# Kernel optimization log

Hardware: AMD Instinct MI355X
Metric: run time of the kernel (lower is better)

Reference implementation:

```python
import jax, jax.numpy as jnp
import numpy as np

B, CIN, H = 8192, 512, 2048  # batch, in_channels, hidden_channels


def _ln(x, g, b, eps=1e-5):
    m = jnp.mean(x, axis=-1, keepdims=True)
    v = jnp.var(x, axis=-1, keepdims=True)
    return (x - m) * jax.lax.rsqrt(v + eps) * g + b


def setup_inputs() -> dict:
    key = jax.random.key(0)
    ks = jax.random.split(key, 16)
    d = {
        'x': jax.random.normal(ks[0], (B, 1, CIN), jnp.float32),
        'h': jax.random.normal(ks[1], (B, H), jnp.float32),
        'c': jax.random.normal(ks[2], (B, H), jnp.float32),
        # input_proj: in_channels -> hidden
        'W_proj': jax.random.normal(ks[3], (H, CIN), jnp.float32) / np.sqrt(CIN),
        'b_proj': jnp.zeros((H,), jnp.float32),
        # layerNorm over concat(x_proj, h) of width 2H
        'g_ln': jnp.ones((2 * H,), jnp.float32),
        'b_ln': jnp.zeros((2 * H,), jnp.float32),
        # cell_norm / hidden_norm
        'g_cn': jnp.ones((H,), jnp.float32),
        'b_cn': jnp.zeros((H,), jnp.float32),
        'g_hn': jnp.ones((H,), jnp.float32),
        'b_hn': jnp.zeros((H,), jnp.float32),
    }
    for name, k in zip(['f', 'i', 'c2', 'o'], ks[4:8]):
        d[f'W_{name}'] = jax.random.normal(k, (H, 2 * H), jnp.float32) / np.sqrt(2 * H)
        d[f'b_{name}'] = jnp.zeros((H,), jnp.float32)
        d[f'g_{name}'] = jnp.ones((H,), jnp.float32)
        d[f'beta_{name}'] = jnp.zeros((H,), jnp.float32)
    return d


def reference(x, h, c, W_proj, b_proj, g_ln, b_ln, g_cn, b_cn, g_hn, b_hn,
              W_f, b_f, g_f, beta_f, W_i, b_i, g_i, beta_i,
              W_c2, b_c2, g_c2, beta_c2, W_o, b_o, g_o, beta_o):
    # x: [B,1,CIN] -> squeeze, project to hidden width (CIN != H branch)
    xp = x[:, 0, :] @ W_proj.T + b_proj                      # [B,H]
    combined = jnp.concatenate([xp, h], axis=-1)             # [B,2H]
    combined = jnp.tanh(_ln(combined, g_ln, b_ln))           # activation = tanh
    # four gate blocks: Linear(2H->H) + LayerNorm (dropout = identity in eval)
    f = jax.nn.sigmoid(_ln(combined @ W_f.T + b_f, g_f, beta_f))
    i = jax.nn.sigmoid(_ln(combined @ W_i.T + b_i, g_i, beta_i))
    o = jax.nn.sigmoid(_ln(combined @ W_o.T + b_o, g_o, beta_o))
    cc = jnp.tanh(_ln(combined @ W_c2.T + b_c2, g_c2, beta_c2))
    next_cell = _ln(f * c + i * cc, g_cn, b_cn)
    next_hidden = jnp.tanh(_ln(o * jnp.tanh(next_cell), g_hn, b_hn))
    # original returns (next_hidden, (next_hidden, next_cell)); stack the two states
    return jnp.stack([next_hidden, next_cell])               # [2,B,H]
```

## Files before the change

kernel.cpp:

```cpp
#include <hip/hip_runtime.h>
#include <stdint.h>


typedef __attribute__((ext_vector_type(8))) short short8;
typedef __attribute__((ext_vector_type(4))) float f32x4;

__device__ __forceinline__ unsigned short f2bf(float x) {
  union { float f; uint32_t u; } v; v.f = x;
  uint32_t r = v.u + 0x7FFFu + ((v.u >> 16) & 1u);
  return (unsigned short)(r >> 16);
}
__device__ __forceinline__ float bf2f(unsigned short u) {
  union { uint32_t u; float f; } v; v.u = ((uint32_t)u) << 16; return v.f;
}
__device__ __forceinline__ void unpack8(uint4 p, float* o) {
  uint32_t w[4] = {p.x, p.y, p.z, p.w};
#pragma unroll
  for (int k = 0; k < 4; k++) {
    o[2*k]   = bf2f((unsigned short)(w[k] & 0xffffu));
    o[2*k+1] = bf2f((unsigned short)(w[k] >> 16));
  }
}
__device__ __forceinline__ uint4 pack8(const float* s) {
  uint4 r;
  r.x = (uint32_t)f2bf(s[0]) | ((uint32_t)f2bf(s[1]) << 16);
  r.y = (uint32_t)f2bf(s[2]) | ((uint32_t)f2bf(s[3]) << 16);
  r.z = (uint32_t)f2bf(s[4]) | ((uint32_t)f2bf(s[5]) << 16);
  r.w = (uint32_t)f2bf(s[6]) | ((uint32_t)f2bf(s[7]) << 16);
  return r;
}
__device__ __forceinline__ float tanh_fast(float x) {
  x = fminf(fmaxf(x, -15.f), 15.f);
  float e = __expf(-2.f * x);
  return (1.f - e) / (1.f + e);
}
__device__ __forceinline__ float sigmoid_fast(float x) {
  return 1.f / (1.f + __expf(-x));
}

__global__ __launch_bounds__(256)
void cvt_all(const float* __restrict__ x, const float* __restrict__ Wp,
             const float* __restrict__ Wf, const float* __restrict__ Wi,
             const float* __restrict__ Wc2, const float* __restrict__ Wo,
             unsigned short* __restrict__ xbf, unsigned short* __restrict__ wpbf,
             unsigned short* __restrict__ Wcat) {
  const int blk = blockIdx.x;
  const float* src;
  unsigned short* dst;
  int i;
  if (blk < 2048) {
    src = x; dst = xbf; i = blk * 256 + threadIdx.x;
  } else if (blk < 2560) {
    src = Wp; dst = wpbf; i = (blk - 2048) * 256 + threadIdx.x;
  } else {
    int b2 = blk - 2560;
    int w = b2 >> 12;
    src = (w == 0) ? Wf : (w == 1) ? Wi : (w == 2) ? Wc2 : Wo;
    dst = Wcat + (size_t)w * 8388608;
    i = (b2 & 4095) * 256 + threadIdx.x;
  }
  const float4* s4 = (const float4*)src;
  float4 a = s4[2*i], b = s4[2*i+1];
  float t[8] = {a.x,a.y,a.z,a.w,b.x,b.y,b.z,b.w};
  ((uint4*)dst)[i] = pack8(t);
}

#define MFMA16(a, b, c) __builtin_amdgcn_mfma_f32_16x16x32_bf16((a), (b), (c), 0, 0, 0)
#define GLDS16(g, l)                                                         \
  __builtin_amdgcn_global_load_lds(                                          \
      (const __attribute__((address_space(1))) void*)(g),                    \
      (__attribute__((address_space(3))) void*)(l), 16, 0, 0)

__global__ __launch_bounds__(512, 2)
void gemm_8ph(const unsigned short* __restrict__ A,
              const unsigned short* __restrict__ Bw,
              const float* __restrict__ b0, const float* __restrict__ b1,
              const float* __restrict__ b2, const float* __restrict__ b3,
              unsigned short* __restrict__ C,
              int M, int N, int K) {
  __shared__ __align__(16) unsigned short As[2][2][128][64];
  __shared__ __align__(16) unsigned short Bs[2][2][128][64];

  const int tid  = threadIdx.x;
  const int lane = tid & 63;
  const int wv   = tid >> 6;
  const int wm   = wv >> 2;
  const int wn   = wv & 3;

  const int nbx = N >> 8;
  const int nwg = (M >> 8) * nbx;
  const int bid = blockIdx.x;
  const int cpx = nwg >> 3;
  const int tile = (nwg & 7) ? bid : (bid & 7) * cpx + (bid >> 3);
  const int bm = (tile / nbx) << 8;
  const int bn = (tile % nbx) << 8;

  const int srow = wv * 8 + (lane >> 3);
  const int schk = (lane & 7) ^ (lane >> 3);
  const unsigned short* ag = A  + (size_t)(bm + srow) * K + schk * 8;
  const unsigned short* bg = Bw + (size_t)(bn + srow) * K + schk * 8;

#define STAGE_A(t, h)                                                        \
  do {                                                                       \
    GLDS16(ag + (size_t)((h) * 128)      * K + (t) * 64,                     \
           &As[(t) & 1][(h)][wv * 8][0]);                                    \
    GLDS16(ag + (size_t)((h) * 128 + 64) * K + (t) * 64,                     \
           &As[(t) & 1][(h)][64 + wv * 8][0]);                               \
  } while (0)
#define STAGE_B(t, h)                                                        \
  do {                                                                       \
    GLDS16(bg + (size_t)((h) * 128)      * K + (t) * 64,                     \
           &Bs[(t) & 1][(h)][wv * 8][0]);                                    \
    GLDS16(bg + (size_t)((h) * 128 + 64) * K + (t) * 64,                     \
           &Bs[(t) & 1][(h)][64 + wv * 8][0]);                               \
  } while (0)

  const int cl = lane & 15, q = lane >> 4;
  const int ard0 = cl * 64 + ((q       ^ (cl & 7)) * 8);
  const int ard1 = cl * 64 + (((4 | q) ^ (cl & 7)) * 8);
  const int brd0 = ((wn & 1) * 64 + cl) * 64 + ((q       ^ (cl & 7)) * 8);
  const int brd1 = ((wn & 1) * 64 + cl) * 64 + (((4 | q) ^ (cl & 7)) * 8);
  const unsigned short* pa0 = &As[0][wm][0][0];
  const unsigned short* pa1 = &As[1][wm][0][0];
  const unsigned short* pb0 = &Bs[0][wn >> 1][0][0];
  const unsigned short* pb1 = &Bs[1][wn >> 1][0][0];

  STAGE_A(0, 0); STAGE_A(0, 1); STAGE_B(0, 0); STAGE_B(0, 1);
  STAGE_A(1, 0);

  f32x4 acc[8][4];
#pragma unroll
  for (int r = 0; r < 8; ++r)
#pragma unroll
    for (int j = 0; j < 4; ++j) acc[r][j] = (f32x4){0.f, 0.f, 0.f, 0.f};

  asm volatile("s_waitcnt vmcnt(2)");
  __builtin_amdgcn_s_barrier();

  short8 af[8], bv[4];
  const int NI = K >> 7;

  for (int i = 0; i < NI; ++i) {
    const int t = 2 * i;
    const bool pf = (i + 1 < NI);

#pragma unroll
    for (int r = 0; r < 8; ++r) af[r] = *(const short8*)(pa0 + ard0 + r * 1024);
    bv[0] = *(const short8*)(pb0 + brd0);
    bv[1] = *(const short8*)(pb0 + brd0 + 1024);
    STAGE_A(t + 1, 1);
    __builtin_amdgcn_s_barrier();
    asm volatile("s_waitcnt lgkmcnt(0)");
    __builtin_amdgcn_s_setprio(1);
#pragma unroll
    for (int r = 0; r < 8; ++r) {
      acc[r][0] = MFMA16(af[r], bv[0], acc[r][0]);
      acc[r][1] = MFMA16(af[r], bv[1], acc[r][1]);
    }
    __builtin_amdgcn_s_setprio(0);
    __builtin_amdgcn_s_barrier();

    bv[2] = *(const short8*)(pb0 + brd0 + 2048);
    bv[3] = *(const short8*)(pb0 + brd0 + 3072);
    STAGE_B(t + 1, 0);
    __builtin_amdgcn_s_barrier();
    asm volatile("s_waitcnt lgkmcnt(0)");
    __builtin_amdgcn_s_setprio(1);
#pragma unroll
    for (int r = 0; r < 8; ++r) {
      acc[r][2] = MFMA16(af[r], bv[2], acc[r][2]);
      acc[r][3] = MFMA16(af[r], bv[3], acc[r][3]);
    }
    __builtin_amdgcn_s_setprio(0);
    __builtin_amdgcn_s_barrier();

#pragma unroll
    for (int r = 0; r < 8; ++r) af[r] = *(const short8*)(pa0 + ard1 + r * 1024);
    bv[0] = *(const short8*)(pb0 + brd1);
    bv[1] = *(const short8*)(pb0 + brd1 + 1024);
    STAGE_B(t + 1, 1);
    __builtin_amdgcn_s_barrier();
    asm volatile("s_waitcnt lgkmcnt(0)");
    __builtin_amdgcn_s_setprio(1);
#pragma unroll
    for (int r = 0; r < 8; ++r) {
      acc[r][0] = MFMA16(af[r], bv[0], acc[r][0]);
      acc[r][1] = MFMA16(af[r], bv[1], acc[r][1]);
    }
    __builtin_amdgcn_s_setprio(0);
    __builtin_amdgcn_s_barrier();

    bv[2] = *(const short8*)(pb0 + brd1 + 2048);
    bv[3] = *(const short8*)(pb0 + brd1 + 3072);
    if (pf) STAGE_A(t + 2, 0);
    __builtin_amdgcn_s_barrier();
    asm volatile("s_waitcnt lgkmcnt(0)");
    __builtin_amdgcn_s_setprio(1);
#pragma unroll
    for (int r = 0; r < 8; ++r) {
      acc[r][2] = MFMA16(af[r], bv[2], acc[r][2]);
      acc[r][3] = MFMA16(af[r], bv[3], acc[r][3]);
    }
    __builtin_amdgcn_s_setprio(0);
    if (pf) { asm volatile("s_waitcnt vmcnt(2)"); }
    else    { asm volatile("s_waitcnt vmcnt(0)"); }
    __builtin_amdgcn_s_barrier();

#pragma unroll
    for (int r = 0; r < 8; ++r) af[r] = *(const short8*)(pa1 + ard0 + r * 1024);
    bv[0] = *(const short8*)(pb1 + brd0);
    bv[1] = *(const short8*)(pb1 + brd0 + 1024);
    if (pf) STAGE_A(t + 2, 1);
    __builtin_amdgcn_s_barrier();
    asm volatile("s_waitcnt lgkmcnt(0)");
    __builtin_amdgcn_s_setprio(1);
#pragma unroll
    for (int r = 0; r < 8; ++r) {
      acc[r][0] = MFMA16(af[r], bv[0], acc[r][0]);
      acc[r][1] = MFMA16(af[r], bv[1], acc[r][1]);
    }
    __builtin_amdgcn_s_setprio(0);
    __builtin_amdgcn_s_barrier();

    bv[2] = *(const short8*)(pb1 + brd0 + 2048);
    bv[3] = *(const short8*)(pb1 + brd0 + 3072);
    if (pf) STAGE_B(t + 2, 0);
    __builtin_amdgcn_s_barrier();
    asm volatile("s_waitcnt lgkmcnt(0)");
    __builtin_amdgcn_s_setprio(1);
#pragma unroll
    for (int r = 0; r < 8; ++r) {
      acc[r][2] = MFMA16(af[r], bv[2], acc[r][2]);
      acc[r][3] = MFMA16(af[r], bv[3], acc[r][3]);
    }
    __builtin_amdgcn_s_setprio(0);
    __builtin_amdgcn_s_barrier();

#pragma unroll
    for (int r = 0; r < 8; ++r) af[r] = *(const short8*)(pa1 + ard1 + r * 1024);
    bv[0] = *(const short8*)(pb1 + brd1);
    bv[1] = *(const short8*)(pb1 + brd1 + 1024);
    if (pf) STAGE_B(t + 2, 1);
    __builtin_amdgcn_s_barrier();
    asm volatile("s_waitcnt lgkmcnt(0)");
    __builtin_amdgcn_s_setprio(1);
#pragma unroll
    for (int r = 0; r < 8; ++r) {
      acc[r][0] = MFMA16(af[r], bv[0], acc[r][0]);
      acc[r][1] = MFMA16(af[r], bv[1], acc[r][1]);
    }
    __builtin_amdgcn_s_setprio(0);
    __builtin_amdgcn_s_barrier();

    bv[2] = *(const short8*)(pb1 + brd1 + 2048);
    bv[3] = *(const short8*)(pb1 + brd1 + 3072);
    if (pf) STAGE_A(t + 3, 0);
    __builtin_amdgcn_s_barrier();
    asm volatile("s_waitcnt lgkmcnt(0)");
    __builtin_amdgcn_s_setprio(1);
#pragma unroll
    for (int r = 0; r < 8; ++r) {
      acc[r][2] = MFMA16(af[r], bv[2], acc[r][2]);
      acc[r][3] = MFMA16(af[r], bv[3], acc[r][3]);
    }
    __builtin_amdgcn_s_setprio(0);
    if (pf) { asm volatile("s_waitcnt vmcnt(2)"); }
    __builtin_amdgcn_s_barrier();
  }

#pragma unroll
  for (int r8 = 0; r8 < 8; ++r8) {
    const int row0 = bm + wm * 128 + r8 * 16 + q * 4;
#pragma unroll
    for (int j = 0; j < 4; ++j) {
      const int col = bn + wn * 64 + j * 16 + cl;
      const int gate = col >> 11;
      const float* bp = (gate == 0) ? b0 : (gate == 1) ? b1 : (gate == 2) ? b2 : b3;
      const float bb = bp[col & 2047];
#pragma unroll
      for (int rr = 0; rr < 4; ++rr)
        C[(size_t)(row0 + rr) * N + col] = f2bf(acc[r8][j][rr] + bb);
    }
  }
}
#undef STAGE_A
#undef STAGE_B

__device__ __forceinline__ float2 block_sum2(float a, float b, float* scr, int t) {
#pragma unroll
  for (int o = 32; o; o >>= 1) { a += __shfl_xor(a, o); b += __shfl_xor(b, o); }
  __syncthreads();
  if ((t & 63) == 0) { scr[(t >> 6) * 2] = a; scr[(t >> 6) * 2 + 1] = b; }
  __syncthreads();
  return make_float2(scr[0] + scr[2] + scr[4] + scr[6],
                     scr[1] + scr[3] + scr[5] + scr[7]);
}

__global__ __launch_bounds__(256)
void ln_tanh_combined(const unsigned short* __restrict__ xp,
                      const float* __restrict__ h,
                      const float* __restrict__ g_ln, const float* __restrict__ b_ln,
                      unsigned short* __restrict__ comb) {
  __shared__ float red[8];
  const int b = blockIdx.x, t = threadIdx.x;
  float xv[8], hv[8];
  unpack8(((const uint4*)(xp + (size_t)b * 2048))[t], xv);
  const float4* hr = (const float4*)(h + (size_t)b * 2048);
  float4 h0 = hr[2*t], h1 = hr[2*t+1];
  hv[0]=h0.x; hv[1]=h0.y; hv[2]=h0.z; hv[3]=h0.w;
  hv[4]=h1.x; hv[5]=h1.y; hv[6]=h1.z; hv[7]=h1.w;
  float s = 0.f, ss = 0.f;
#pragma unroll
  for (int e = 0; e < 8; e++) {
    s += xv[e] + hv[e];
    ss += xv[e]*xv[e] + hv[e]*hv[e];
  }
  float2 r = block_sum2(s, ss, red, t);
  float mean = r.x * (1.f/4096.f);
  float var  = r.y * (1.f/4096.f) - mean*mean;
  float rs = rsqrtf(var + 1e-5f);
  float o0[8], o1[8];
  const int j0 = t * 8;
#pragma unroll
  for (int e = 0; e < 8; e++) {
    int j = j0 + e;
    o0[e] = tanh_fast((xv[e] - mean) * rs * g_ln[j] + b_ln[j]);
  }
#pragma unroll
  for (int e = 0; e < 8; e++) {
    int j = 2048 + j0 + e;
    o1[e] = tanh_fast((hv[e] - mean) * rs * g_ln[j] + b_ln[j]);
  }
  uint4* cr = (uint4*)(comb + (size_t)b * 4096);
  cr[t] = pack8(o0);
  cr[256 + t] = pack8(o1);
}

__global__ __launch_bounds__(256)
void finalize(const unsigned short* __restrict__ gates, const float* __restrict__ c,
              const float* __restrict__ g_f,  const float* __restrict__ bt_f,
              const float* __restrict__ g_i,  const float* __restrict__ bt_i,
              const float* __restrict__ g_c2, const float* __restrict__ bt_c2,
              const float* __restrict__ g_o,  const float* __restrict__ bt_o,
              const float* __restrict__ g_cn, const float* __restrict__ b_cn,
              const float* __restrict__ g_hn, const float* __restrict__ b_hn,
              float* __restrict__ out) {
  __shared__ float red32[32];
  const int b = blockIdx.x, t = threadIdx.x;
  const unsigned short* gr = gates + (size_t)b * 8192;
  float fv[8], iv[8], c2v[8], ov[8];
  unpack8(((const uint4*)(gr        ))[t], fv);
  unpack8(((const uint4*)(gr + 2048))[t], iv);
  unpack8(((const uint4*)(gr + 4096))[t], c2v);
  unpack8(((const uint4*)(gr + 6144))[t], ov);

  float s[8] = {0,0,0,0,0,0,0,0};
#pragma unroll
  for (int e = 0; e < 8; e++) {
    s[0] += fv[e];  s[1] += fv[e]*fv[e];
    s[2] += iv[e];  s[3] += iv[e]*iv[e];
    s[4] += c2v[e]; s[5] += c2v[e]*c2v[e];
    s[6] += ov[e];  s[7] += ov[e]*ov[e];
  }
#pragma unroll
  for (int o = 32; o; o >>= 1)
#pragma unroll
    for (int q2 = 0; q2 < 8; q2++) s[q2] += __shfl_xor(s[q2], o);
  if ((t & 63) == 0) {
#pragma unroll
    for (int q2 = 0; q2 < 8; q2++) red32[(t >> 6) * 8 + q2] = s[q2];
  }
  __syncthreads();
#pragma unroll
  for (int q2 = 0; q2 < 8; q2++)
    s[q2] = red32[q2] + red32[8 + q2] + red32[16 + q2] + red32[24 + q2];

  const float inv = 1.f / 2048.f;
  float m_f = s[0]*inv, rs_f = rsqrtf(s[1]*inv - m_f*m_f + 1e-5f);
  float m_i = s[2]*inv, rs_i = rsqrtf(s[3]*inv - m_i*m_i + 1e-5f);
  float m_c = s[4]*inv, rs_c = rsqrtf(s[5]*inv - m_c*m_c + 1e-5f);
  float m_o = s[6]*inv, rs_o = rsqrtf(s[7]*inv - m_o*m_o + 1e-5f);

  const int j0 = t * 8;
  float cv[8];
  const float4* crp = (const float4*)(c + (size_t)b * 2048);
  float4 c0 = crp[2*t], c1 = crp[2*t+1];
  cv[0]=c0.x; cv[1]=c0.y; cv[2]=c0.z; cv[3]=c0.w;
  cv[4]=c1.x; cv[5]=c1.y; cv[6]=c1.z; cv[7]=c1.w;

  float cellraw[8], os[8];
  float s2 = 0.f, ss2 = 0.f;
#pragma unroll
  for (int e = 0; e < 8; e++) {
    int j = j0 + e;
    float fgate = sigmoid_fast((fv[e]  - m_f) * rs_f * g_f[j]  + bt_f[j]);
    float igate = sigmoid_fast((iv[e]  - m_i) * rs_i * g_i[j]  + bt_i[j]);
    float cgate = tanh_fast   ((c2v[e] - m_c) * rs_c * g_c2[j] + bt_c2[j]);
    os[e]       = sigmoid_fast((ov[e]  - m_o) * rs_o * g_o[j]  + bt_o[j]);
    cellraw[e] = fgate * cv[e] + igate * cgate;
    s2 += cellraw[e]; ss2 += cellraw[e]*cellraw[e];
  }
  float2 rc = block_sum2(s2, ss2, red32, t);
  float m2 = rc.x * inv, rs2 = rsqrtf(rc.y * inv - m2*m2 + 1e-5f);

  float nc[8], hraw[8];
  float s3 = 0.f, ss3 = 0.f;
#pragma unroll
  for (int e = 0; e < 8; e++) {
    int j = j0 + e;
    nc[e] = (cellraw[e] - m2) * rs2 * g_cn[j] + b_cn[j];
    hraw[e] = os[e] * tanh_fast(nc[e]);
    s3 += hraw[e]; ss3 += hraw[e]*hraw[e];
  }
  float2 rh = block_sum2(s3, ss3, red32, t);
  float m3 = rh.x * inv, rs3 = rsqrtf(rh.y * inv - m3*m3 + 1e-5f);

  float nh[8];
#pragma unroll
  for (int e = 0; e < 8; e++) {
    int j = j0 + e;
    nh[e] = tanh_fast((hraw[e] - m3) * rs3 * g_hn[j] + b_hn[j]);
  }
  float4* oh = (float4*)(out + (size_t)b * 2048 + j0);
  oh[0] = make_float4(nh[0], nh[1], nh[2], nh[3]);
  oh[1] = make_float4(nh[4], nh[5], nh[6], nh[7]);
  float4* oc = (float4*)(out + 16777216ull + (size_t)b * 2048 + j0);
  oc[0] = make_float4(nc[0], nc[1], nc[2], nc[3]);
  oc[1] = make_float4(nc[4], nc[5], nc[6], nc[7]);
}

extern "C" void kernel_launch(void* const* d_in, const int* in_sizes, int n_in,
                              void* d_out, int out_size, void* d_ws, size_t ws_size,
                              hipStream_t stream) {
  const float* x      = (const float*)d_in[0];
  const float* h      = (const float*)d_in[1];
  const float* c      = (const float*)d_in[2];
  const float* W_proj = (const float*)d_in[3];
  const float* b_proj = (const float*)d_in[4];
  const float* g_ln   = (const float*)d_in[5];
  const float* b_ln   = (const float*)d_in[6];
  const float* g_cn   = (const float*)d_in[7];
  const float* b_cn   = (const float*)d_in[8];
  const float* g_hn   = (const float*)d_in[9];
  const float* b_hn   = (const float*)d_in[10];
  const float* W_f    = (const float*)d_in[11];
  const float* b_f    = (const float*)d_in[12];
  const float* g_f    = (const float*)d_in[13];
  const float* bt_f   = (const float*)d_in[14];
  const float* W_i    = (const float*)d_in[15];
  const float* b_i    = (const float*)d_in[16];
  const float* g_i    = (const float*)d_in[17];
  const float* bt_i   = (const float*)d_in[18];
  const float* W_c2   = (const float*)d_in[19];
  const float* b_c2   = (const float*)d_in[20];
  const float* g_c2   = (const float*)d_in[21];
  const float* bt_c2  = (const float*)d_in[22];
  const float* W_o    = (const float*)d_in[23];
  const float* b_o    = (const float*)d_in[24];
  const float* g_o    = (const float*)d_in[25];
  const float* bt_o   = (const float*)d_in[26];
  float* out = (float*)d_out;
  char* ws = (char*)d_ws;

  unsigned short* Wcat  = (unsigned short*)(ws);
  unsigned short* comb  = (unsigned short*)(ws + 67108864ull);
  unsigned short* gates = (unsigned short*)(ws + 134217728ull);
  unsigned short* xbf   = (unsigned short*)(ws + 134217728ull);
  unsigned short* wpbf  = (unsigned short*)(ws + 142606336ull);
  unsigned short* xpbf  = (unsigned short*)(ws + 144703488ull);

  cvt_all<<<18944, 256, 0, stream>>>(x, W_proj, W_f, W_i, W_c2, W_o,
                                     xbf, wpbf, Wcat);

  gemm_8ph<<<dim3(256), dim3(512), 0, stream>>>(
      xbf, wpbf, b_proj, b_proj, b_proj, b_proj, xpbf, 8192, 2048, 512);

  ln_tanh_combined<<<8192, 256, 0, stream>>>(xpbf, h, g_ln, b_ln, comb);

  gemm_8ph<<<dim3(1024), dim3(512), 0, stream>>>(
      comb, Wcat, b_f, b_i, b_c2, b_o, gates, 8192, 8192, 4096);

  finalize<<<8192, 256, 0, stream>>>(gates, c, g_f, bt_f, g_i, bt_i, g_c2, bt_c2,
                                     g_o, bt_o, g_cn, b_cn, g_hn, b_hn, out);
}
```

Before: 1.036 ms.

## Split GEMM LDS staging into K-halves for deeper finer-grained prefetch

The LDS tiles are reorganized from [row-half][128][64] to [k-half][256][32]. Each stage now loads a 32-wide K slice for all 256 rows, with a matching XOR swizzle adapted to 4 chunks per row. The prologue and main loop issue loads further ahead (vmcnt 10), so each MFMA phase waits only on the K-slice it consumes rather than on a whole row-half. This aims to hide global-load latency better, at the cost of more outstanding loads, a different bank-conflict pattern and more complex waitcnt bookkeeping.

```diff
diff --git a/kernel.cpp b/kernel.cpp
--- a/kernel.cpp
+++ b/kernel.cpp
@@ -78,8 +78,8 @@
               const float* __restrict__ b2, const float* __restrict__ b3,
               unsigned short* __restrict__ C,
               int M, int N, int K) {
-  __shared__ __align__(16) unsigned short As[2][2][128][64];
-  __shared__ __align__(16) unsigned short Bs[2][2][128][64];
+  __shared__ __align__(16) unsigned short As[2][2][256][32];
+  __shared__ __align__(16) unsigned short Bs[2][2][256][32];
 
   const int tid  = threadIdx.x;
   const int lane = tid & 63;
@@ -95,38 +95,41 @@
   const int bm = (tile / nbx) << 8;
   const int bn = (tile % nbx) << 8;
 
-  const int srow = wv * 8 + (lane >> 3);
-  const int schk = (lane & 7) ^ (lane >> 3);
+  const int srow = wv * 16 + (lane >> 2);
+  const int schk = (lane & 3) ^ ((lane >> 3) & 3);
   const unsigned short* ag = A  + (size_t)(bm + srow) * K + schk * 8;
   const unsigned short* bg = Bw + (size_t)(bn + srow) * K + schk * 8;
 
-#define STAGE_A(t, h)                                                        \
+#define STAGE_A(t, ks)                                                       \
   do {                                                                       \
-    GLDS16(ag + (size_t)((h) * 128)      * K + (t) * 64,                     \
-           &As[(t) & 1][(h)][wv * 8][0]);                                    \
-    GLDS16(ag + (size_t)((h) * 128 + 64) * K + (t) * 64,                     \
-           &As[(t) & 1][(h)][64 + wv * 8][0]);                               \
+    GLDS16(ag + (size_t)(t) * 64 + (ks) * 32,                                \
+           &As[(t) & 1][(ks)][wv * 16][0]);                                  \
+    GLDS16(ag + (size_t)128 * K + (size_t)(t) * 64 + (ks) * 32,              \
+           &As[(t) & 1][(ks)][128 + wv * 16][0]);                            \
   } while (0)
-#define STAGE_B(t, h)                                                        \
+#define STAGE_B(t, ks)                                                       \
   do {                                                                       \
-    GLDS16(bg + (size_t)((h) * 128)      * K + (t) * 64,                     \
-           &Bs[(t) & 1][(h)][wv * 8][0]);                                    \
-    GLDS16(bg + (size_t)((h) * 128 + 64) * K + (t) * 64,                     \
-           &Bs[(t) & 1][(h)][64 + wv * 8][0]);                               \
+    GLDS16(bg + (size_t)(t) * 64 + (ks) * 32,                                \
+           &Bs[(t) & 1][(ks)][wv * 16][0]);                                  \
+    GLDS16(bg + (size_t)128 * K + (size_t)(t) * 64 + (ks) * 32,              \
+           &Bs[(t) & 1][(ks)][128 + wv * 16][0]);                            \
   } while (0)
 
   const int cl = lane & 15, q = lane >> 4;
-  const int ard0 = cl * 64 + ((q       ^ (cl & 7)) * 8);
-  const int ard1 = cl * 64 + (((4 | q) ^ (cl & 7)) * 8);
-  const int brd0 = ((wn & 1) * 64 + cl) * 64 + ((q       ^ (cl & 7)) * 8);
-  const int brd1 = ((wn & 1) * 64 + cl) * 64 + (((4 | q) ^ (cl & 7)) * 8);
-  const unsigned short* pa0 = &As[0][wm][0][0];
-  const unsigned short* pa1 = &As[1][wm][0][0];
-  const unsigned short* pb0 = &Bs[0][wn >> 1][0][0];
-  const unsigned short* pb1 = &Bs[1][wn >> 1][0][0];
-
-  STAGE_A(0, 0); STAGE_A(0, 1); STAGE_B(0, 0); STAGE_B(0, 1);
-  STAGE_A(1, 0);
+  const int fcl = (cl >> 1) & 3;
+  const int ard = (wm * 128 + cl) * 32 + ((q ^ fcl) * 8);
+  const int brd = (wn * 64 + cl) * 32 + ((q ^ fcl) * 8);
+  const unsigned short* pA00 = &As[0][0][0][0] + ard;
+  const unsigned short* pA01 = &As[0][1][0][0] + ard;
+  const unsigned short* pA10 = &As[1][0][0][0] + ard;
+  const unsigned short* pA11 = &As[1][1][0][0] + ard;
+  const unsigned short* pB00 = &Bs[0][0][0][0] + brd;
+  const unsigned short* pB01 = &Bs[0][1][0][0] + brd;
+  const unsigned short* pB10 = &Bs[1][0][0][0] + brd;
+  const unsigned short* pB11 = &Bs[1][1][0][0] + brd;
+
+  STAGE_A(0, 0); STAGE_B(0, 0); STAGE_A(0, 1); STAGE_B(0, 1);
+  STAGE_A(1, 0); STAGE_B(1, 0); STAGE_A(1, 1);
 
   f32x4 acc[8][4];
 #pragma unroll
@@ -134,7 +137,7 @@
 #pragma unroll
     for (int j = 0; j < 4; ++j) acc[r][j] = (f32x4){0.f, 0.f, 0.f, 0.f};
 
-  asm volatile("s_waitcnt vmcnt(2)");
+  asm volatile("s_waitcnt vmcnt(10)");
   __builtin_amdgcn_s_barrier();
 
   short8 af[8], bv[4];
@@ -145,10 +148,10 @@
     const bool pf = (i + 1 < NI);
 
 #pragma unroll
-    for (int r = 0; r < 8; ++r) af[r] = *(const short8*)(pa0 + ard0 + r * 1024);
-    bv[0] = *(const short8*)(pb0 + brd0);
-    bv[1] = *(const short8*)(pb0 + brd0 + 1024);
-    STAGE_A(t + 1, 1);
+    for (int r = 0; r < 8; ++r) af[r] = *(const short8*)(pA00 + r * 512);
+    bv[0] = *(const short8*)(pB00);
+    bv[1] = *(const short8*)(pB00 + 512);
+    STAGE_B(t + 1, 1);
     __builtin_amdgcn_s_barrier();
     asm volatile("s_waitcnt lgkmcnt(0)");
     __builtin_amdgcn_s_setprio(1);
@@ -160,9 +163,9 @@
     __builtin_amdgcn_s_setprio(0);
     __builtin_amdgcn_s_barrier();
 
-    bv[2] = *(const short8*)(pb0 + brd0 + 2048);
-    bv[3] = *(const short8*)(pb0 + brd0 + 3072);
-    STAGE_B(t + 1, 0);
+    bv[2] = *(const short8*)(pB00 + 1024);
+    bv[3] = *(const short8*)(pB00 + 1536);
+    if (pf) STAGE_A(t + 2, 0);
     __builtin_amdgcn_s_barrier();
     asm volatile("s_waitcnt lgkmcnt(0)");
     __builtin_amdgcn_s_setprio(1);
@@ -172,13 +175,15 @@
       acc[r][3] = MFMA16(af[r], bv[3], acc[r][3]);
     }
     __builtin_amdgcn_s_setprio(0);
-    __builtin_amdgcn_s_barrier();
-
-#pragma unroll
-    for (int r = 0; r < 8; ++r) af[r] = *(const short8*)(pa0 + ard1 + r * 1024);
-    bv[0] = *(const short8*)(pb0 + brd1);
-    bv[1] = *(const short8*)(pb0 + brd1 + 1024);
-    STAGE_B(t + 1, 1);
+    if (pf) { asm volatile("s_waitcnt vmcnt(10)"); }
+    else    { asm volatile("s_waitcnt vmcnt(8)");  }
+    __builtin_amdgcn_s_barrier();
+
+#pragma unroll
+    for (int r = 0; r < 8; ++r) af[r] = *(const short8*)(pA01 + r * 512);
+    bv[0] = *(const short8*)(pB01);
+    bv[1] = *(const short8*)(pB01 + 512);
+    if (pf) STAGE_B(t + 2, 0);
     __builtin_amdgcn_s_barrier();
     asm volatile("s_waitcnt lgkmcnt(0)");
     __builtin_amdgcn_s_setprio(1);
@@ -190,9 +195,9 @@
     __builtin_amdgcn_s_setprio(0);
     __builtin_amdgcn_s_barrier();
 
-    bv[2] = *(const short8*)(pb0 + brd1 + 2048);
-    bv[3] = *(const short8*)(pb0 + brd1 + 3072);
-    if (pf) STAGE_A(t + 2, 0);
+    bv[2] = *(const short8*)(pB01 + 1024);
+    bv[3] = *(const short8*)(pB01 + 1536);
+    if (pf) STAGE_A(t + 2, 1);
     __builtin_amdgcn_s_barrier();
     asm volatile("s_waitcnt lgkmcnt(0)");
     __builtin_amdgcn_s_setprio(1);
@@ -202,15 +207,15 @@
       acc[r][3] = MFMA16(af[r], bv[3], acc[r][3]);
     }
     __builtin_amdgcn_s_setprio(0);
-    if (pf) { asm volatile("s_waitcnt vmcnt(2)"); }
-    else    { asm volatile("s_waitcnt vmcnt(0)"); }
-    __builtin_amdgcn_s_barrier();
-
-#pragma unroll
-    for (int r = 0; r < 8; ++r) af[r] = *(const short8*)(pa1 + ard0 + r * 1024);
-    bv[0] = *(const short8*)(pb1 + brd0);
-    bv[1] = *(const short8*)(pb1 + brd0 + 1024);
-    if (pf) STAGE_A(t + 2, 1);
+    if (pf) { asm volatile("s_waitcnt vmcnt(10)"); }
+    else    { asm volatile("s_waitcnt vmcnt(4)");  }
+    __builtin_amdgcn_s_barrier();
+
+#pragma unroll
+    for (int r = 0; r < 8; ++r) af[r] = *(const short8*)(pA10 + r * 512);
+    bv[0] = *(const short8*)(pB10);
+    bv[1] = *(const short8*)(pB10 + 512);
+    if (pf) STAGE_B(t + 2, 1);
     __builtin_amdgcn_s_barrier();
     asm volatile("s_waitcnt lgkmcnt(0)");
     __builtin_amdgcn_s_setprio(1);
@@ -222,9 +227,9 @@
     __builtin_amdgcn_s_setprio(0);
     __builtin_amdgcn_s_barrier();
 
-    bv[2] = *(const short8*)(pb1 + brd0 + 2048);
-    bv[3] = *(const short8*)(pb1 + brd0 + 3072);
-    if (pf) STAGE_B(t + 2, 0);
+    bv[2] = *(const short8*)(pB10 + 1024);
+    bv[3] = *(const short8*)(pB10 + 1536);
+    if (pf) STAGE_A(t + 3, 0);
     __builtin_amdgcn_s_barrier();
     asm volatile("s_waitcnt lgkmcnt(0)");
     __builtin_amdgcn_s_setprio(1);
@@ -234,13 +239,15 @@
       acc[r][3] = MFMA16(af[r], bv[3], acc[r][3]);
     }
     __builtin_amdgcn_s_setprio(0);
-    __builtin_amdgcn_s_barrier();
-
-#pragma unroll
-    for (int r = 0; r < 8; ++r) af[r] = *(const short8*)(pa1 + ard1 + r * 1024);
-    bv[0] = *(const short8*)(pb1 + brd1);
-    bv[1] = *(const short8*)(pb1 + brd1 + 1024);
-    if (pf) STAGE_B(t + 2, 1);
+    if (pf) { asm volatile("s_waitcnt vmcnt(10)"); }
+    else    { asm volatile("s_waitcnt vmcnt(0)");  }
+    __builtin_amdgcn_s_barrier();
+
+#pragma unroll
+    for (int r = 0; r < 8; ++r) af[r] = *(const short8*)(pA11 + r * 512);
+    bv[0] = *(const short8*)(pB11);
+    bv[1] = *(const short8*)(pB11 + 512);
+    if (pf) STAGE_B(t + 3, 0);
     __builtin_amdgcn_s_barrier();
     asm volatile("s_waitcnt lgkmcnt(0)");
     __builtin_amdgcn_s_setprio(1);
@@ -252,9 +259,9 @@
     __builtin_amdgcn_s_setprio(0);
     __builtin_amdgcn_s_barrier();
 
-    bv[2] = *(const short8*)(pb1 + brd1 + 2048);
-    bv[3] = *(const short8*)(pb1 + brd1 + 3072);
-    if (pf) STAGE_A(t + 3, 0);
+    bv[2] = *(const short8*)(pB11 + 1024);
+    bv[3] = *(const short8*)(pB11 + 1536);
+    if (pf) STAGE_A(t + 3, 1);
     __builtin_amdgcn_s_barrier();
     asm volatile("s_waitcnt lgkmcnt(0)");
     __builtin_amdgcn_s_setprio(1);
@@ -264,7 +271,7 @@
       acc[r][3] = MFMA16(af[r], bv[3], acc[r][3]);
     }
     __builtin_amdgcn_s_setprio(0);
-    if (pf) { asm volatile("s_waitcnt vmcnt(2)"); }
+    if (pf) { asm volatile("s_waitcnt vmcnt(10)"); }
     __builtin_amdgcn_s_barrier();
   }
 
```

New measurement: 930.4 us. 10.2% less time.
